# Performance work log

Measured on AMD Instinct MI355X. Metric: run time of the kernel, lower is better.

Reference implementation:

```python
import jax, jax.numpy as jnp
import numpy as np

N_MQ = 50000   # number of 'mq' (user/query) nodes
N_SQ = 50000   # number of 'sq' (movie/sub-query) nodes
E = 600000     # edges of type ('mq','queries','sq'); reverse edges are the flip
EL = 200000    # supervision edges for the classifier
H = 128        # hidden_channels
F_IN = 768     # raw 'sq' feature dim (movie_lin in_features)
N_LAYERS = 4


def setup_inputs() -> dict:
    key = jax.random.key(0)
    ks = jax.random.split(key, 12)
    sH = 1.0 / np.sqrt(H)
    sF = 1.0 / np.sqrt(F_IN)
    return {
        "mq_node_id": jnp.arange(N_MQ, dtype=jnp.int64) if jax.config.jax_enable_x64 else jnp.arange(N_MQ, dtype=jnp.int32),
        "sq_node_id": jnp.arange(N_SQ, dtype=jnp.int32),
        "sq_x": jax.random.normal(ks[0], (N_SQ, F_IN), jnp.float32),
        "edge_index": jax.random.randint(ks[1], (2, E), 0, N_SQ),
        "edge_label_index": jax.random.randint(ks[2], (2, EL), 0, N_SQ),
        "user_emb": jax.random.normal(ks[3], (N_MQ, H), jnp.float32) * 0.1,
        "movie_emb": jax.random.normal(ks[4], (N_SQ, H), jnp.float32) * 0.1,
        "lin_W": jax.random.normal(ks[5], (H, F_IN), jnp.float32) * sF,
        "lin_b": jnp.zeros((H,), jnp.float32),
        "Wl_s": jax.random.normal(ks[6], (N_LAYERS, H, H), jnp.float32) * sH,
        "bl_s": jnp.zeros((N_LAYERS, H), jnp.float32),
        "Wr_s": jax.random.normal(ks[7], (N_LAYERS, H, H), jnp.float32) * sH,
        "Wl_m": jax.random.normal(ks[8], (N_LAYERS, H, H), jnp.float32) * sH,
        "bl_m": jnp.zeros((N_LAYERS, H), jnp.float32),
        "Wr_m": jax.random.normal(ks[9], (N_LAYERS, H, H), jnp.float32) * sH,
    }


def _sage(x_src, x_dst, src_idx, dst_idx, Wl, bl, Wr, n_dst):
    """PyG SAGEConv (aggr='mean', root_weight=True, bias on lin_l only)."""
    msg = x_src[src_idx]                                     # [E, H] gather
    agg = jax.ops.segment_sum(msg, dst_idx, num_segments=n_dst)
    cnt = jax.ops.segment_sum(jnp.ones((src_idx.shape[0], 1), x_src.dtype),
                              dst_idx, num_segments=n_dst)
    mean = agg / jnp.maximum(cnt, 1.0)                       # mean over in-neighbors
    return mean @ Wl.T + bl + x_dst @ Wr.T


def reference(mq_node_id, sq_node_id, sq_x, edge_index, edge_label_index,
              user_emb, movie_emb, lin_W, lin_b,
              Wl_s, bl_s, Wr_s, Wl_m, bl_m, Wr_m):
    # input encoders
    x_mq = user_emb[mq_node_id]                              # [N_MQ, H]
    x_sq = sq_x @ lin_W.T + lin_b + movie_emb[sq_node_id]    # [N_SQ, H]
    src, dst = edge_index[0], edge_index[1]                  # mq -> sq; reverse is flip
    for i in range(N_LAYERS):
        new_sq = _sage(x_mq, x_sq, src, dst, Wl_s[i], bl_s[i], Wr_s[i], N_SQ)
        new_mq = _sage(x_sq, x_mq, dst, src, Wl_m[i], bl_m[i], Wr_m[i], N_MQ)
        if i == 0:  # only conv1 has ReLU in the original GNN
            new_sq = jax.nn.relu(new_sq)
            new_mq = jax.nn.relu(new_mq)
        x_mq, x_sq = new_mq, new_sq
    # dot-product classifier over supervision edges
    return (x_mq[edge_label_index[0]] * x_sq[edge_label_index[1]]).sum(axis=-1)
```

## Files before the change

### kernel.cpp

```cpp
#include <hip/hip_runtime.h>

#define H    128
#define NMQ  50000
#define NSQ  50000
#define NE   600000
#define NEL  200000
#define FIN  768
#define NLAYERS 4
#define NBLK (NSQ / 16)

typedef __attribute__((ext_vector_type(8))) short bf16x8;
typedef __attribute__((ext_vector_type(4))) float f32x4;

__device__ inline ushort f2b(float f) {
  unsigned u = __float_as_uint(f);
  u = (u + 0x7FFFu + ((u >> 16) & 1u)) >> 16;
  return (ushort)u;
}
__device__ inline float b2f(ushort h) { return __uint_as_float((unsigned)h << 16); }

__global__ void cvt_bf16(const float* __restrict__ in, ushort* __restrict__ out, int n4) {
  int i = blockIdx.x * blockDim.x + threadIdx.x;
  if (i >= n4) return;
  float4 v = ((const float4*)in)[i];
  ushort4 o;
  o.x = f2b(v.x); o.y = f2b(v.y); o.z = f2b(v.z); o.w = f2b(v.w);
  ((ushort4*)out)[i] = o;
}

__global__ void cvt_w5(const float* __restrict__ linW,
                       const float* __restrict__ Wls, const float* __restrict__ Wrs,
                       const float* __restrict__ Wlm, const float* __restrict__ Wrm,
                       ushort* olinW, ushort* oWls, ushort* oWrs, ushort* oWlm, ushort* oWrm) {
  const float* in; ushort* out; int n4;
  switch (blockIdx.y) {
    case 0: in = linW; out = olinW; n4 = H * FIN / 4; break;
    case 1: in = Wls;  out = oWls;  n4 = NLAYERS * H * H / 4; break;
    case 2: in = Wrs;  out = oWrs;  n4 = NLAYERS * H * H / 4; break;
    case 3: in = Wlm;  out = oWlm;  n4 = NLAYERS * H * H / 4; break;
    default: in = Wrm; out = oWrm;  n4 = NLAYERS * H * H / 4; break;
  }
  int i = blockIdx.x * blockDim.x + threadIdx.x;
  if (i >= n4) return;
  float4 v = ((const float4*)in)[i];
  ushort4 o;
  o.x = f2b(v.x); o.y = f2b(v.y); o.z = f2b(v.z); o.w = f2b(v.w);
  ((ushort4*)out)[i] = o;
}

__global__ __launch_bounds__(64) void encoder_mfma(
    const float* __restrict__ A, const ushort* __restrict__ Wb,
    const float* __restrict__ bias, const float* __restrict__ memb,
    ushort* __restrict__ C)
{
  int lane = threadIdx.x;
  int rowbase = blockIdx.x * 16;
  int t = lane >> 4, fr = lane & 15;
  f32x4 acc[8];
  #pragma unroll
  for (int c = 0; c < 8; ++c)
    #pragma unroll
    for (int q = 0; q < 4; ++q) acc[c][q] = 0.f;

  int arow = rowbase + fr;
  const float* Abase = A + (long)arow * FIN + t * 8;

  for (int k0 = 0; k0 < FIN; k0 += 32) {
    bf16x8 af, bfm[8];
    {
      const float* p = Abase + k0;
      float4 v0 = *(const float4*)p;
      float4 v1 = *(const float4*)(p + 4);
      ushort tmp[8];
      tmp[0] = f2b(v0.x); tmp[1] = f2b(v0.y); tmp[2] = f2b(v0.z); tmp[3] = f2b(v0.w);
      tmp[4] = f2b(v1.x); tmp[5] = f2b(v1.y); tmp[6] = f2b(v1.z); tmp[7] = f2b(v1.w);
      af = *(bf16x8*)tmp;
    }
    #pragma unroll
    for (int cc = 0; cc < 8; ++cc) {
      int col = cc * 16 + fr;
      bfm[cc] = *(const bf16x8*)(Wb + (long)col * FIN + k0 + t * 8);
    }
    #pragma unroll
    for (int cc = 0; cc < 8; ++cc)
      acc[cc] = __builtin_amdgcn_mfma_f32_16x16x32_bf16(af, bfm[cc], acc[cc], 0, 0, 0);
  }
  #pragma unroll
  for (int cc = 0; cc < 8; ++cc)
    #pragma unroll
    for (int q = 0; q < 4; ++q) {
      int row = rowbase + t * 4 + q;
      int col = cc * 16 + fr;
      float v = acc[cc][q] + bias[col] + memb[(long)row * H + col];
      C[(long)row * H + col] = f2b(v);
    }
}

__global__ __launch_bounds__(64) void fused_layer2(
    const ushort* __restrict__ xmq, const ushort* __restrict__ xsq,
    const int* __restrict__ offs_f, const int* __restrict__ csr_f,
    const int* __restrict__ offs_r, const int* __restrict__ csr_r,
    const ushort* __restrict__ Wls, const ushort* __restrict__ Wrs,
    const float* __restrict__ bls,
    const ushort* __restrict__ Wlm, const ushort* __restrict__ Wrm,
    const float* __restrict__ blm,
    ushort* __restrict__ nsq, ushort* __restrict__ nmq, int relu)
{
  __shared__ ushort mtile[16 * 128];
  int side = blockIdx.x >= NBLK;
  int bidx = side ? blockIdx.x - NBLK : blockIdx.x;
  const ushort* xg   = side ? xsq    : xmq;
  const ushort* xs   = side ? xmq    : xsq;
  const int*    offs = side ? offs_r : offs_f;
  const int*    csr  = side ? csr_r  : csr_f;
  const ushort* Wl   = side ? Wlm    : Wls;
  const ushort* Wr   = side ? Wrm    : Wrs;
  const float*  bias = side ? blm    : bls;
  ushort*       Cout = side ? nmq    : nsq;

  int lane = threadIdx.x;
  int rowbase = bidx * 16;
  int t = lane >> 4, fr = lane & 15;
  const unsigned* X = (const unsigned*)xg;

  int srow = rowbase + fr;
  bf16x8 sfrag[4];
  #pragma unroll
  for (int ks = 0; ks < 4; ++ks)
    sfrag[ks] = *(const bf16x8*)(xs + (long)srow * H + (ks * 4 + t) * 8);

  int wslot = lane >> 2;
  unsigned* mt32 = (unsigned*)mtile;
  for (int i = 0; i < 16; ++i) {
    int row = rowbase + i;
    int s = offs[row], e = offs[row + 1];
    float a0 = 0.f, a1 = 0.f;
    int j = s;
    for (; j + 8 <= e; j += 8) {
      long i0 = csr[j], i1 = csr[j+1], i2 = csr[j+2], i3 = csr[j+3];
      long i4 = csr[j+4], i5 = csr[j+5], i6 = csr[j+6], i7 = csr[j+7];
      unsigned x0 = X[i0*64+lane], x1 = X[i1*64+lane], x2 = X[i2*64+lane], x3 = X[i3*64+lane];
      unsigned x4 = X[i4*64+lane], x5 = X[i5*64+lane], x6 = X[i6*64+lane], x7 = X[i7*64+lane];
      a0 += b2f((ushort)(x0 & 0xffff)) + b2f((ushort)(x1 & 0xffff))
          + b2f((ushort)(x2 & 0xffff)) + b2f((ushort)(x3 & 0xffff))
          + b2f((ushort)(x4 & 0xffff)) + b2f((ushort)(x5 & 0xffff))
          + b2f((ushort)(x6 & 0xffff)) + b2f((ushort)(x7 & 0xffff));
      a1 += b2f((ushort)(x0 >> 16)) + b2f((ushort)(x1 >> 16))
          + b2f((ushort)(x2 >> 16)) + b2f((ushort)(x3 >> 16))
          + b2f((ushort)(x4 >> 16)) + b2f((ushort)(x5 >> 16))
          + b2f((ushort)(x6 >> 16)) + b2f((ushort)(x7 >> 16));
    }
    if (j + 4 <= e) {
      long i0 = csr[j], i1 = csr[j+1], i2 = csr[j+2], i3 = csr[j+3];
      unsigned x0 = X[i0*64+lane], x1 = X[i1*64+lane], x2 = X[i2*64+lane], x3 = X[i3*64+lane];
      a0 += b2f((ushort)(x0 & 0xffff)) + b2f((ushort)(x1 & 0xffff))
          + b2f((ushort)(x2 & 0xffff)) + b2f((ushort)(x3 & 0xffff));
      a1 += b2f((ushort)(x0 >> 16)) + b2f((ushort)(x1 >> 16))
          + b2f((ushort)(x2 >> 16)) + b2f((ushort)(x3 >> 16));
      j += 4;
    }
    for (; j < e; ++j) {
      unsigned x = X[(long)csr[j] * 64 + lane];
      a0 += b2f((ushort)(x & 0xffff));
      a1 += b2f((ushort)(x >> 16));
    }
    float inv = (e > s) ? 1.f / (float)(e - s) : 0.f;
    a0 *= inv; a1 *= inv;
    int sw = (wslot & 8) | ((wslot & 7) ^ (i & 7));
    mt32[i * 64 + sw * 4 + (lane & 3)] = (unsigned)f2b(a0) | ((unsigned)f2b(a1) << 16);
  }

  f32x4 acc[8];
  #pragma unroll
  for (int c = 0; c < 8; ++c)
    #pragma unroll
    for (int q = 0; q < 4; ++q) acc[c][q] = 0.f;

  #pragma unroll
  for (int ks = 0; ks < 4; ++ks) {
    int slot = ks * 4 + t;
    int sw = (slot & 8) | ((slot & 7) ^ (fr & 7));
    bf16x8 af = *(const bf16x8*)&mtile[fr * 128 + sw * 8];
    bf16x8 bfm[8];
    #pragma unroll
    for (int cc = 0; cc < 8; ++cc) {
      int col = cc * 16 + fr;
      bfm[cc] = *(const bf16x8*)(Wl + (long)col * H + slot * 8);
    }
    #pragma unroll
    for (int cc = 0; cc < 8; ++cc)
      acc[cc] = __builtin_amdgcn_mfma_f32_16x16x32_bf16(af, bfm[cc], acc[cc], 0, 0, 0);
  }
  #pragma unroll
  for (int ks = 0; ks < 4; ++ks) {
    int slot = ks * 4 + t;
    bf16x8 bfm[8];
    #pragma unroll
    for (int cc = 0; cc < 8; ++cc) {
      int col = cc * 16 + fr;
      bfm[cc] = *(const bf16x8*)(Wr + (long)col * H + slot * 8);
    }
    #pragma unroll
    for (int cc = 0; cc < 8; ++cc)
      acc[cc] = __builtin_amdgcn_mfma_f32_16x16x32_bf16(sfrag[ks], bfm[cc], acc[cc], 0, 0, 0);
  }
  #pragma unroll
  for (int cc = 0; cc < 8; ++cc)
    #pragma unroll
    for (int q = 0; q < 4; ++q) {
      int row = rowbase + t * 4 + q;
      int col = cc * 16 + fr;
      float v = acc[cc][q] + bias[col];
      if (relu) v = fmaxf(v, 0.f);
      Cout[(long)row * H + col] = f2b(v);
    }
}

__global__ void deg_count(const int* __restrict__ eidx, int* __restrict__ df, int* __restrict__ dr) {
  int e = blockIdx.x * blockDim.x + threadIdx.x;
  if (e >= NE) return;
  atomicAdd(dr + eidx[e], 1);
  atomicAdd(df + eidx[NE + e], 1);
}

__global__ __launch_bounds__(1024) void exscan2(
    const int* __restrict__ degf, const int* __restrict__ degr,
    int* __restrict__ offf, int* __restrict__ offr)
{
  __shared__ int part[1024];
  const int* deg = blockIdx.x ? degr : degf;
  int* offs = blockIdx.x ? offr : offf;
  int n = blockIdx.x ? NMQ : NSQ;
  int t = threadIdx.x;
  int chunk = (n + 1023) >> 10;
  int beg = t * chunk, end = beg + chunk;
  if (end > n) end = n;
  int s = 0;
  for (int i = beg; i < end; ++i) s += deg[i];
  part[t] = s;
  __syncthreads();
  for (int offd = 1; offd < 1024; offd <<= 1) {
    int v = 0;
    if (t >= offd) v = part[t - offd];
    __syncthreads();
    part[t] += v;
    __syncthreads();
  }
  int run = (t == 0) ? 0 : part[t - 1];
  for (int i = beg; i < end; ++i) { offs[i] = run; run += deg[i]; }
  if (t == 1023) offs[n] = part[1023];
}

__global__ void csr_fill(const int* __restrict__ eidx,
                         const int* __restrict__ offs_f, const int* __restrict__ offs_r,
                         int* __restrict__ cur_f, int* __restrict__ cur_r,
                         int* __restrict__ csr_f, int* __restrict__ csr_r) {
  int e = blockIdx.x * blockDim.x + threadIdx.x;
  if (e >= NE) return;
  int s = eidx[e], d = eidx[NE + e];
  int p = atomicAdd(cur_f + d, 1); csr_f[offs_f[d] + p] = s;
  int q = atomicAdd(cur_r + s, 1); csr_r[offs_r[s] + q] = d;
}

__global__ __launch_bounds__(256) void edge_dot_b(
    const ushort* __restrict__ xmq, const ushort* __restrict__ xsq,
    const int* __restrict__ eli, float* __restrict__ out)
{
  int wid = (blockIdx.x << 2) + (threadIdx.x >> 6);
  int lane = threadIdx.x & 63;
  if (wid >= NEL) return;
  int a = eli[wid], b = eli[NEL + wid];
  unsigned xa = ((const unsigned*)xmq)[(long)a * 64 + lane];
  unsigned xb = ((const unsigned*)xsq)[(long)b * 64 + lane];
  float p = b2f((ushort)(xa & 0xffff)) * b2f((ushort)(xb & 0xffff))
          + b2f((ushort)(xa >> 16))    * b2f((ushort)(xb >> 16));
  #pragma unroll
  for (int off = 32; off; off >>= 1) p += __shfl_down(p, off, 64);
  if (lane == 0) out[wid] = p;
}

extern "C" void kernel_launch(void* const* d_in, const int* in_sizes, int n_in,
                              void* d_out, int out_size, void* d_ws, size_t ws_size,
                              hipStream_t stream) {
  (void)in_sizes; (void)n_in; (void)out_size; (void)ws_size;
  const float* sq_x      = (const float*)d_in[2];
  const int*   eidx      = (const int*)d_in[3];
  const int*   eli       = (const int*)d_in[4];
  const float* user_emb  = (const float*)d_in[5];
  const float* movie_emb = (const float*)d_in[6];
  const float* lin_W     = (const float*)d_in[7];
  const float* lin_b     = (const float*)d_in[8];
  const float* Wl_s      = (const float*)d_in[9];
  const float* bl_s      = (const float*)d_in[10];
  const float* Wr_s      = (const float*)d_in[11];
  const float* Wl_m      = (const float*)d_in[12];
  const float* bl_m      = (const float*)d_in[13];
  const float* Wr_m      = (const float*)d_in[14];
  float* out = (float*)d_out;

  char* ws = (char*)d_ws;
  size_t off = 0;
  auto alloc = [&](size_t bytes) {
    char* p = ws + off;
    off += (bytes + 255) & ~(size_t)255;
    return p;
  };
  ushort* xmq_a = (ushort*)alloc((size_t)NMQ * H * 2);
  ushort* xmq_b = (ushort*)alloc((size_t)NMQ * H * 2);
  ushort* xsq_a = (ushort*)alloc((size_t)NSQ * H * 2);
  ushort* xsq_b = (ushort*)alloc((size_t)NSQ * H * 2);
  ushort* linWb = (ushort*)alloc((size_t)H * FIN * 2);
  ushort* Wlsb  = (ushort*)alloc((size_t)NLAYERS * H * H * 2);
  ushort* Wrsb  = (ushort*)alloc((size_t)NLAYERS * H * H * 2);
  ushort* Wlmb  = (ushort*)alloc((size_t)NLAYERS * H * H * 2);
  ushort* Wrmb  = (ushort*)alloc((size_t)NLAYERS * H * H * 2);
  int* deg_f  = (int*)alloc((size_t)NSQ * 4);
  int* deg_r  = (int*)alloc((size_t)NMQ * 4);
  int* cur_f  = (int*)alloc((size_t)NSQ * 4);
  int* cur_r  = (int*)alloc((size_t)NMQ * 4);
  int* offs_f = (int*)alloc((size_t)(NSQ + 1) * 4);
  int* offs_r = (int*)alloc((size_t)(NMQ + 1) * 4);
  int* csr_f  = (int*)alloc((size_t)NE * 4);
  int* csr_r  = (int*)alloc((size_t)NE * 4);

  hipMemsetAsync(deg_f, 0, (char*)offs_f - (char*)deg_f, stream);

  cvt_bf16<<<(NMQ * H / 4 + 255) / 256, 256, 0, stream>>>(user_emb, xmq_a, NMQ * H / 4);
  cvt_w5<<<dim3((H * FIN / 4 + 255) / 256, 5), 256, 0, stream>>>(
      lin_W, Wl_s, Wr_s, Wl_m, Wr_m, linWb, Wlsb, Wrsb, Wlmb, Wrmb);

  encoder_mfma<<<NSQ / 16, 64, 0, stream>>>(sq_x, linWb, lin_b, movie_emb, xsq_a);
  deg_count<<<(NE + 255) / 256, 256, 0, stream>>>(eidx, deg_f, deg_r);
  exscan2<<<2, 1024, 0, stream>>>(deg_f, deg_r, offs_f, offs_r);
  csr_fill<<<(NE + 255) / 256, 256, 0, stream>>>(eidx, offs_f, offs_r, cur_f, cur_r, csr_f, csr_r);

  ushort *cm = xmq_a, *cs = xsq_a, *nm = xmq_b, *ns = xsq_b;
  for (int l = 0; l < NLAYERS; ++l) {
    fused_layer2<<<2 * NBLK, 64, 0, stream>>>(cm, cs, offs_f, csr_f, offs_r, csr_r,
        Wlsb + (size_t)l * H * H, Wrsb + (size_t)l * H * H, bl_s + (size_t)l * H,
        Wlmb + (size_t)l * H * H, Wrmb + (size_t)l * H * H, bl_m + (size_t)l * H,
        ns, nm, l == 0);
    ushort* t;
    t = cm; cm = nm; nm = t;
    t = cs; cs = ns; ns = t;
  }
  edge_dot_b<<<(NEL + 3) / 4, 256, 0, stream>>>(cm, cs, eli, out);
}
```

Before: 724.8 us.

## Flatten block edge list and double-buffer neighbor gathers; prefetch encoder A loads

The per-row neighbor loop in the fused layer kernel is replaced by one flat pass over the block's whole CSR range. Gathers are issued 16 at a time into two alternating register buffers, and a new per-edge destination-row array tracks row boundaries and writes each row's mean when the row changes. This is meant to keep many independent loads in flight across row boundaries instead of stalling on rows with few neighbors, at the cost of extra register pressure and an extra array read per edge. The encoder also software-prefetches the next fp32 A fragment before each MFMA step.

```diff
diff --git a/kernel.cpp b/kernel.cpp
--- a/kernel.cpp
+++ b/kernel.cpp
@@ -63,28 +63,40 @@
     for (int q = 0; q < 4; ++q) acc[c][q] = 0.f;
 
   int arow = rowbase + fr;
-  const float* Abase = A + (long)arow * FIN + t * 8;
-
-  for (int k0 = 0; k0 < FIN; k0 += 32) {
-    bf16x8 af, bfm[8];
-    {
-      const float* p = Abase + k0;
-      float4 v0 = *(const float4*)p;
-      float4 v1 = *(const float4*)(p + 4);
-      ushort tmp[8];
-      tmp[0] = f2b(v0.x); tmp[1] = f2b(v0.y); tmp[2] = f2b(v0.z); tmp[3] = f2b(v0.w);
-      tmp[4] = f2b(v1.x); tmp[5] = f2b(v1.y); tmp[6] = f2b(v1.z); tmp[7] = f2b(v1.w);
-      af = *(bf16x8*)tmp;
-    }
-    #pragma unroll
-    for (int cc = 0; cc < 8; ++cc) {
-      int col = cc * 16 + fr;
-      bfm[cc] = *(const bf16x8*)(Wb + (long)col * FIN + k0 + t * 8);
-    }
-    #pragma unroll
-    for (int cc = 0; cc < 8; ++cc)
-      acc[cc] = __builtin_amdgcn_mfma_f32_16x16x32_bf16(af, bfm[cc], acc[cc], 0, 0, 0);
-  }
+  const float* Ab = A + (long)arow * FIN + t * 8;
+
+#define ENC_COMPUTE(k0, c0, c1) do {                                        \
+    ushort tmp[8];                                                          \
+    tmp[0] = f2b((c0).x); tmp[1] = f2b((c0).y);                             \
+    tmp[2] = f2b((c0).z); tmp[3] = f2b((c0).w);                             \
+    tmp[4] = f2b((c1).x); tmp[5] = f2b((c1).y);                             \
+    tmp[6] = f2b((c1).z); tmp[7] = f2b((c1).w);                             \
+    bf16x8 af = *(bf16x8*)tmp;                                              \
+    bf16x8 bfm[8];                                                          \
+    _Pragma("unroll")                                                       \
+    for (int cc = 0; cc < 8; ++cc) {                                        \
+      int col = cc * 16 + fr;                                               \
+      bfm[cc] = *(const bf16x8*)(Wb + (long)col * FIN + (k0) + t * 8);      \
+    }                                                                       \
+    _Pragma("unroll")                                                       \
+    for (int cc = 0; cc < 8; ++cc)                                          \
+      acc[cc] = __builtin_amdgcn_mfma_f32_16x16x32_bf16(af, bfm[cc], acc[cc], 0, 0, 0); \
+  } while (0)
+
+  float4 u0 = *(const float4*)Ab;
+  float4 u1 = *(const float4*)(Ab + 4);
+  for (int ki = 0; ki < FIN / 32; ki += 2) {
+    float4 v0 = *(const float4*)(Ab + (ki + 1) * 32);
+    float4 v1 = *(const float4*)(Ab + (ki + 1) * 32 + 4);
+    ENC_COMPUTE(ki * 32, u0, u1);
+    if (ki + 2 < FIN / 32) {
+      u0 = *(const float4*)(Ab + (ki + 2) * 32);
+      u1 = *(const float4*)(Ab + (ki + 2) * 32 + 4);
+    }
+    ENC_COMPUTE((ki + 1) * 32, v0, v1);
+  }
+#undef ENC_COMPUTE
+
   #pragma unroll
   for (int cc = 0; cc < 8; ++cc)
     #pragma unroll
@@ -99,7 +111,9 @@
 __global__ __launch_bounds__(64) void fused_layer2(
     const ushort* __restrict__ xmq, const ushort* __restrict__ xsq,
     const int* __restrict__ offs_f, const int* __restrict__ csr_f,
+    const int* __restrict__ drow_f,
     const int* __restrict__ offs_r, const int* __restrict__ csr_r,
+    const int* __restrict__ drow_r,
     const ushort* __restrict__ Wls, const ushort* __restrict__ Wrs,
     const float* __restrict__ bls,
     const ushort* __restrict__ Wlm, const ushort* __restrict__ Wrm,
@@ -113,6 +127,7 @@
   const ushort* xs   = side ? xmq    : xsq;
   const int*    offs = side ? offs_r : offs_f;
   const int*    csr  = side ? csr_r  : csr_f;
+  const int*    drow = side ? drow_r : drow_f;
   const ushort* Wl   = side ? Wlm    : Wls;
   const ushort* Wr   = side ? Wrm    : Wrs;
   const float*  bias = side ? blm    : bls;
@@ -131,44 +146,74 @@
 
   int wslot = lane >> 2;
   unsigned* mt32 = (unsigned*)mtile;
-  for (int i = 0; i < 16; ++i) {
-    int row = rowbase + i;
-    int s = offs[row], e = offs[row + 1];
-    float a0 = 0.f, a1 = 0.f;
-    int j = s;
-    for (; j + 8 <= e; j += 8) {
-      long i0 = csr[j], i1 = csr[j+1], i2 = csr[j+2], i3 = csr[j+3];
-      long i4 = csr[j+4], i5 = csr[j+5], i6 = csr[j+6], i7 = csr[j+7];
-      unsigned x0 = X[i0*64+lane], x1 = X[i1*64+lane], x2 = X[i2*64+lane], x3 = X[i3*64+lane];
-      unsigned x4 = X[i4*64+lane], x5 = X[i5*64+lane], x6 = X[i6*64+lane], x7 = X[i7*64+lane];
-      a0 += b2f((ushort)(x0 & 0xffff)) + b2f((ushort)(x1 & 0xffff))
-          + b2f((ushort)(x2 & 0xffff)) + b2f((ushort)(x3 & 0xffff))
-          + b2f((ushort)(x4 & 0xffff)) + b2f((ushort)(x5 & 0xffff))
-          + b2f((ushort)(x6 & 0xffff)) + b2f((ushort)(x7 & 0xffff));
-      a1 += b2f((ushort)(x0 >> 16)) + b2f((ushort)(x1 >> 16))
-          + b2f((ushort)(x2 >> 16)) + b2f((ushort)(x3 >> 16))
-          + b2f((ushort)(x4 >> 16)) + b2f((ushort)(x5 >> 16))
-          + b2f((ushort)(x6 >> 16)) + b2f((ushort)(x7 >> 16));
-    }
-    if (j + 4 <= e) {
-      long i0 = csr[j], i1 = csr[j+1], i2 = csr[j+2], i3 = csr[j+3];
-      unsigned x0 = X[i0*64+lane], x1 = X[i1*64+lane], x2 = X[i2*64+lane], x3 = X[i3*64+lane];
-      a0 += b2f((ushort)(x0 & 0xffff)) + b2f((ushort)(x1 & 0xffff))
-          + b2f((ushort)(x2 & 0xffff)) + b2f((ushort)(x3 & 0xffff));
-      a1 += b2f((ushort)(x0 >> 16)) + b2f((ushort)(x1 >> 16))
-          + b2f((ushort)(x2 >> 16)) + b2f((ushort)(x3 >> 16));
-      j += 4;
-    }
-    for (; j < e; ++j) {
-      unsigned x = X[(long)csr[j] * 64 + lane];
-      a0 += b2f((ushort)(x & 0xffff));
-      a1 += b2f((ushort)(x >> 16));
-    }
-    float inv = (e > s) ? 1.f / (float)(e - s) : 0.f;
-    a0 *= inv; a1 *= inv;
-    int sw = (wslot & 8) | ((wslot & 7) ^ (i & 7));
-    mt32[i * 64 + sw * 4 + (lane & 3)] = (unsigned)f2b(a0) | ((unsigned)f2b(a1) << 16);
-  }
+  #pragma unroll
+  for (int i = 0; i < 16; ++i) mt32[i * 64 + lane] = 0;
+
+  int cbeg = offs[rowbase], cend = offs[rowbase + 16];
+  float a0 = 0.f, a1 = 0.f;
+  int cur = -1, cnt = 0;
+
+#define GISSUE(ax, rx, c0, nn) do {                                         \
+    if ((nn) == 16) {                                                       \
+      _Pragma("unroll")                                                     \
+      for (int j = 0; j < 16; ++j) {                                        \
+        rx[j] = drow[(c0) + j];                                             \
+        ax[j] = X[(long)csr[(c0) + j] * 64 + lane];                         \
+      }                                                                     \
+    } else {                                                                \
+      _Pragma("unroll")                                                     \
+      for (int j = 0; j < 16; ++j) if (j < (nn)) {                          \
+        rx[j] = drow[(c0) + j];                                             \
+        ax[j] = X[(long)csr[(c0) + j] * 64 + lane];                         \
+      }                                                                     \
+    } } while (0)
+
+#define GCONSUME(ax, rx, nn) do {                                           \
+    _Pragma("unroll")                                                       \
+    for (int j = 0; j < 16; ++j) if (j < (nn)) {                            \
+      int rowj = rx[j];                                                     \
+      if (rowj != cur) {                                                    \
+        if (cnt > 0) {                                                      \
+          float inv = 1.f / (float)cnt;                                     \
+          int sw = (wslot & 8) | ((wslot & 7) ^ (cur & 7));                 \
+          mt32[(cur & 15) * 64 + sw * 4 + (lane & 3)] =                     \
+              (unsigned)f2b(a0 * inv) | ((unsigned)f2b(a1 * inv) << 16);    \
+        }                                                                   \
+        cur = rowj; a0 = 0.f; a1 = 0.f; cnt = 0;                            \
+      }                                                                     \
+      unsigned w = ax[j];                                                   \
+      a0 += b2f((ushort)(w & 0xffff));                                      \
+      a1 += b2f((ushort)(w >> 16));                                         \
+      ++cnt;                                                                \
+    } } while (0)
+
+  {
+    unsigned aA[16], aB[16];
+    int rA[16], rB[16];
+    int c = cbeg;
+    int nA = cend - c; if (nA > 16) nA = 16;
+    if (nA > 0) GISSUE(aA, rA, c, nA);
+    c += nA;
+    while (nA > 0) {
+      int nB = cend - c; if (nB > 16) nB = 16;
+      if (nB > 0) GISSUE(aB, rB, c, nB);
+      c += nB;
+      GCONSUME(aA, rA, nA);
+      if (nB == 0) break;
+      nA = cend - c; if (nA > 16) nA = 16;
+      if (nA > 0) GISSUE(aA, rA, c, nA);
+      c += nA;
+      GCONSUME(aB, rB, nB);
+    }
+    if (cnt > 0) {
+      float inv = 1.f / (float)cnt;
+      int sw = (wslot & 8) | ((wslot & 7) ^ (cur & 7));
+      mt32[(cur & 15) * 64 + sw * 4 + (lane & 3)] =
+          (unsigned)f2b(a0 * inv) | ((unsigned)f2b(a1 * inv) << 16);
+    }
+  }
+#undef GISSUE
+#undef GCONSUME
 
   f32x4 acc[8];
   #pragma unroll
@@ -254,12 +299,13 @@
 __global__ void csr_fill(const int* __restrict__ eidx,
                          const int* __restrict__ offs_f, const int* __restrict__ offs_r,
                          int* __restrict__ cur_f, int* __restrict__ cur_r,
-                         int* __restrict__ csr_f, int* __restrict__ csr_r) {
+                         int* __restrict__ csr_f, int* __restrict__ csr_r,
+                         int* __restrict__ drow_f, int* __restrict__ drow_r) {
   int e = blockIdx.x * blockDim.x + threadIdx.x;
   if (e >= NE) return;
   int s = eidx[e], d = eidx[NE + e];
-  int p = atomicAdd(cur_f + d, 1); csr_f[offs_f[d] + p] = s;
-  int q = atomicAdd(cur_r + s, 1); csr_r[offs_r[s] + q] = d;
+  int p = atomicAdd(cur_f + d, 1); int pf = offs_f[d] + p; csr_f[pf] = s; drow_f[pf] = d;
+  int q = atomicAdd(cur_r + s, 1); int pr = offs_r[s] + q; csr_r[pr] = d; drow_r[pr] = s;
 }
 
 __global__ __launch_bounds__(256) void edge_dot_b(
@@ -322,6 +368,8 @@
   int* offs_r = (int*)alloc((size_t)(NMQ + 1) * 4);
   int* csr_f  = (int*)alloc((size_t)NE * 4);
   int* csr_r  = (int*)alloc((size_t)NE * 4);
+  int* drow_f = (int*)alloc((size_t)NE * 4);
+  int* drow_r = (int*)alloc((size_t)NE * 4);
 
   hipMemsetAsync(deg_f, 0, (char*)offs_f - (char*)deg_f, stream);
 
@@ -332,11 +380,13 @@
   encoder_mfma<<<NSQ / 16, 64, 0, stream>>>(sq_x, linWb, lin_b, movie_emb, xsq_a);
   deg_count<<<(NE + 255) / 256, 256, 0, stream>>>(eidx, deg_f, deg_r);
   exscan2<<<2, 1024, 0, stream>>>(deg_f, deg_r, offs_f, offs_r);
-  csr_fill<<<(NE + 255) / 256, 256, 0, stream>>>(eidx, offs_f, offs_r, cur_f, cur_r, csr_f, csr_r);
+  csr_fill<<<(NE + 255) / 256, 256, 0, stream>>>(eidx, offs_f, offs_r, cur_f, cur_r,
+                                                 csr_f, csr_r, drow_f, drow_r);
 
   ushort *cm = xmq_a, *cs = xsq_a, *nm = xmq_b, *ns = xsq_b;
   for (int l = 0; l < NLAYERS; ++l) {
-    fused_layer2<<<2 * NBLK, 64, 0, stream>>>(cm, cs, offs_f, csr_f, offs_r, csr_r,
+    fused_layer2<<<2 * NBLK, 64, 0, stream>>>(cm, cs,
+        offs_f, csr_f, drow_f, offs_r, csr_r, drow_r,
         Wlsb + (size_t)l * H * H, Wrsb + (size_t)l * H * H, bl_s + (size_t)l * H,
         Wlmb + (size_t)l * H * H, Wrmb + (size_t)l * H * H, bl_m + (size_t)l * H,
         ns, nm, l == 0);
```

Result: faster. 700.8 us (-3.3%).

## Pack CSR into padded groups of four and gather with 16-lane vector loads

Applied to the files above, without the earlier changes.

Changes the CSR build so each destination's neighbor list is padded into groups of four slots, with a group-to-row array. The aggregation loop then processes a block's 16 rows as one stream of groups. Each quarter-wave gathers a full 256-byte row with bf16x8 loads, the loads are double-buffered across banks of four groups, and partial sums are reduced with cross-lane shuffles. This targets the per-row serial loop and the 4-byte-per-lane gathers. In exchange it adds padding work for masked slots, a second scan, extra memset and metadata buffers, and a fixed NGMAX capacity that depends on the degree distribution.

```diff
diff --git a/kernel.cpp b/kernel.cpp
--- a/kernel.cpp
+++ b/kernel.cpp
@@ -8,6 +8,8 @@
 #define FIN  768
 #define NLAYERS 4
 #define NBLK (NSQ / 16)
+#define NGMAX 188000
+#define PCMAX (NGMAX * 4)
 
 typedef __attribute__((ext_vector_type(8))) short bf16x8;
 typedef __attribute__((ext_vector_type(4))) float f32x4;
@@ -68,9 +70,9 @@
   for (int k0 = 0; k0 < FIN; k0 += 32) {
     bf16x8 af, bfm[8];
     {
-      const float* p = Abase + k0;
-      float4 v0 = *(const float4*)p;
-      float4 v1 = *(const float4*)(p + 4);
+      const float* pp = Abase + k0;
+      float4 v0 = *(const float4*)pp;
+      float4 v1 = *(const float4*)(pp + 4);
       ushort tmp[8];
       tmp[0] = f2b(v0.x); tmp[1] = f2b(v0.y); tmp[2] = f2b(v0.z); tmp[3] = f2b(v0.w);
       tmp[4] = f2b(v1.x); tmp[5] = f2b(v1.y); tmp[6] = f2b(v1.z); tmp[7] = f2b(v1.w);
@@ -98,8 +100,10 @@
 
 __global__ __launch_bounds__(64) void fused_layer2(
     const ushort* __restrict__ xmq, const ushort* __restrict__ xsq,
-    const int* __restrict__ offs_f, const int* __restrict__ csr_f,
-    const int* __restrict__ offs_r, const int* __restrict__ csr_r,
+    const int* __restrict__ offs_f, const int* __restrict__ goff_f,
+    const int* __restrict__ pcsr_f, const int* __restrict__ grow_f,
+    const int* __restrict__ offs_r, const int* __restrict__ goff_r,
+    const int* __restrict__ pcsr_r, const int* __restrict__ grow_r,
     const ushort* __restrict__ Wls, const ushort* __restrict__ Wrs,
     const float* __restrict__ bls,
     const ushort* __restrict__ Wlm, const ushort* __restrict__ Wrm,
@@ -112,63 +116,99 @@
   const ushort* xg   = side ? xsq    : xmq;
   const ushort* xs   = side ? xmq    : xsq;
   const int*    offs = side ? offs_r : offs_f;
-  const int*    csr  = side ? csr_r  : csr_f;
+  const int*    goff = side ? goff_r : goff_f;
+  const int*    pcsr = side ? pcsr_r : pcsr_f;
+  const int*    grow = side ? grow_r : grow_f;
   const ushort* Wl   = side ? Wlm    : Wls;
   const ushort* Wr   = side ? Wrm    : Wrs;
   const float*  bias = side ? blm    : bls;
   ushort*       Cout = side ? nmq    : nsq;
 
   int lane = threadIdx.x;
+  int ep = lane >> 4;
+  int ch = lane & 15;
   int rowbase = bidx * 16;
+
   int t = lane >> 4, fr = lane & 15;
-  const unsigned* X = (const unsigned*)xg;
-
   int srow = rowbase + fr;
   bf16x8 sfrag[4];
   #pragma unroll
   for (int ks = 0; ks < 4; ++ks)
     sfrag[ks] = *(const bf16x8*)(xs + (long)srow * H + (ks * 4 + t) * 8);
 
-  int wslot = lane >> 2;
   unsigned* mt32 = (unsigned*)mtile;
-  for (int i = 0; i < 16; ++i) {
-    int row = rowbase + i;
-    int s = offs[row], e = offs[row + 1];
-    float a0 = 0.f, a1 = 0.f;
-    int j = s;
-    for (; j + 8 <= e; j += 8) {
-      long i0 = csr[j], i1 = csr[j+1], i2 = csr[j+2], i3 = csr[j+3];
-      long i4 = csr[j+4], i5 = csr[j+5], i6 = csr[j+6], i7 = csr[j+7];
-      unsigned x0 = X[i0*64+lane], x1 = X[i1*64+lane], x2 = X[i2*64+lane], x3 = X[i3*64+lane];
-      unsigned x4 = X[i4*64+lane], x5 = X[i5*64+lane], x6 = X[i6*64+lane], x7 = X[i7*64+lane];
-      a0 += b2f((ushort)(x0 & 0xffff)) + b2f((ushort)(x1 & 0xffff))
-          + b2f((ushort)(x2 & 0xffff)) + b2f((ushort)(x3 & 0xffff))
-          + b2f((ushort)(x4 & 0xffff)) + b2f((ushort)(x5 & 0xffff))
-          + b2f((ushort)(x6 & 0xffff)) + b2f((ushort)(x7 & 0xffff));
-      a1 += b2f((ushort)(x0 >> 16)) + b2f((ushort)(x1 >> 16))
-          + b2f((ushort)(x2 >> 16)) + b2f((ushort)(x3 >> 16))
-          + b2f((ushort)(x4 >> 16)) + b2f((ushort)(x5 >> 16))
-          + b2f((ushort)(x6 >> 16)) + b2f((ushort)(x7 >> 16));
-    }
-    if (j + 4 <= e) {
-      long i0 = csr[j], i1 = csr[j+1], i2 = csr[j+2], i3 = csr[j+3];
-      unsigned x0 = X[i0*64+lane], x1 = X[i1*64+lane], x2 = X[i2*64+lane], x3 = X[i3*64+lane];
-      a0 += b2f((ushort)(x0 & 0xffff)) + b2f((ushort)(x1 & 0xffff))
-          + b2f((ushort)(x2 & 0xffff)) + b2f((ushort)(x3 & 0xffff));
-      a1 += b2f((ushort)(x0 >> 16)) + b2f((ushort)(x1 >> 16))
-          + b2f((ushort)(x2 >> 16)) + b2f((ushort)(x3 >> 16));
-      j += 4;
-    }
-    for (; j < e; ++j) {
-      unsigned x = X[(long)csr[j] * 64 + lane];
-      a0 += b2f((ushort)(x & 0xffff));
-      a1 += b2f((ushort)(x >> 16));
-    }
-    float inv = (e > s) ? 1.f / (float)(e - s) : 0.f;
-    a0 *= inv; a1 *= inv;
-    int sw = (wslot & 8) | ((wslot & 7) ^ (i & 7));
-    mt32[i * 64 + sw * 4 + (lane & 3)] = (unsigned)f2b(a0) | ((unsigned)f2b(a1) << 16);
-  }
+  #pragma unroll
+  for (int i = 0; i < 16; ++i) mt32[i * 64 + lane] = 0;
+
+  float acc8[8];
+  #pragma unroll
+  for (int q = 0; q < 8; ++q) acc8[q] = 0.f;
+  int cur = -1;
+
+  int gbeg = goff[rowbase], gend = goff[rowbase + 16];
+  int gn = gend - gbeg;
+
+#define FLUSH() do {                                                        \
+    if (cur >= 0) {                                                         \
+      _Pragma("unroll")                                                     \
+      for (int q = 0; q < 8; ++q) {                                         \
+        acc8[q] += __shfl_xor(acc8[q], 16, 64);                             \
+        acc8[q] += __shfl_xor(acc8[q], 32, 64);                             \
+      }                                                                     \
+      int s0 = offs[cur], e0 = offs[cur + 1];                               \
+      float inv = (e0 > s0) ? 1.f / (float)(e0 - s0) : 0.f;                 \
+      if (ep == 0) {                                                        \
+        ushort tmp[8];                                                      \
+        _Pragma("unroll")                                                   \
+        for (int q = 0; q < 8; ++q) tmp[q] = f2b(acc8[q] * inv);            \
+        int sw = (ch & 8) | ((ch & 7) ^ (cur & 7));                         \
+        *(bf16x8*)&mtile[(cur & 15) * 128 + sw * 8] = *(bf16x8*)tmp;        \
+      }                                                                     \
+      _Pragma("unroll")                                                     \
+      for (int q = 0; q < 8; ++q) acc8[q] = 0.f;                            \
+    } } while (0)
+
+#define LOADBANK(vv, mm, rr, g0) do {                                       \
+    _Pragma("unroll")                                                       \
+    for (int k = 0; k < 4; ++k) {                                           \
+      int gg = (g0) + k;                                                    \
+      int ggs = gg < gend ? gg : gbeg;                                      \
+      int si = pcsr[ggs * 4 + ep];                                          \
+      mm[k] = si >= 0 ? 1.f : 0.f;                                          \
+      long rsafe = si >= 0 ? si : 0;                                        \
+      vv[k] = *(const bf16x8*)(xg + rsafe * H + ch * 8);                    \
+      rr[k] = grow[ggs];                                                    \
+    } } while (0)
+
+#define CONSUMEBANK(vv, mm, rr, g0) do {                                    \
+    _Pragma("unroll")                                                       \
+    for (int k = 0; k < 4; ++k) {                                           \
+      int gg = (g0) + k;                                                    \
+      if (gg < gend) {                                                      \
+        int rnow = rr[k];                                                   \
+        if (rnow != cur) { FLUSH(); cur = rnow; }                           \
+        _Pragma("unroll")                                                   \
+        for (int q = 0; q < 8; ++q)                                         \
+          acc8[q] = fmaf(mm[k], b2f((ushort)vv[k][q]), acc8[q]);            \
+      }                                                                     \
+    } } while (0)
+
+  if (gn > 0) {
+    bf16x8 vA[4], vB[4];
+    float mA[4], mB[4];
+    int rA[4], rB[4];
+    LOADBANK(vA, mA, rA, gbeg);
+    for (int base = 0; base < gn; base += 8) {
+      LOADBANK(vB, mB, rB, gbeg + base + 4);
+      CONSUMEBANK(vA, mA, rA, gbeg + base);
+      LOADBANK(vA, mA, rA, gbeg + base + 8);
+      CONSUMEBANK(vB, mB, rB, gbeg + base + 4);
+    }
+    FLUSH();
+  }
+#undef FLUSH
+#undef LOADBANK
+#undef CONSUMEBANK
 
   f32x4 acc[8];
   #pragma unroll
@@ -225,41 +265,70 @@
 
 __global__ __launch_bounds__(1024) void exscan2(
     const int* __restrict__ degf, const int* __restrict__ degr,
-    int* __restrict__ offf, int* __restrict__ offr)
+    int* __restrict__ offf, int* __restrict__ offr,
+    int* __restrict__ gofff, int* __restrict__ goffr)
 {
   __shared__ int part[1024];
   const int* deg = blockIdx.x ? degr : degf;
   int* offs = blockIdx.x ? offr : offf;
+  int* goffs = blockIdx.x ? goffr : gofff;
   int n = blockIdx.x ? NMQ : NSQ;
   int t = threadIdx.x;
   int chunk = (n + 1023) >> 10;
   int beg = t * chunk, end = beg + chunk;
   if (end > n) end = n;
-  int s = 0;
-  for (int i = beg; i < end; ++i) s += deg[i];
-  part[t] = s;
+
+  {
+    int s = 0;
+    for (int i = beg; i < end; ++i) s += deg[i];
+    part[t] = s;
+    __syncthreads();
+    for (int offd = 1; offd < 1024; offd <<= 1) {
+      int v = 0;
+      if (t >= offd) v = part[t - offd];
+      __syncthreads();
+      part[t] += v;
+      __syncthreads();
+    }
+    int run = (t == 0) ? 0 : part[t - 1];
+    for (int i = beg; i < end; ++i) { offs[i] = run; run += deg[i]; }
+    if (t == 1023) offs[n] = part[1023];
+  }
   __syncthreads();
-  for (int offd = 1; offd < 1024; offd <<= 1) {
-    int v = 0;
-    if (t >= offd) v = part[t - offd];
+  {
+    int s = 0;
+    for (int i = beg; i < end; ++i) s += (deg[i] + 3) >> 2;
+    part[t] = s;
     __syncthreads();
-    part[t] += v;
-    __syncthreads();
-  }
-  int run = (t == 0) ? 0 : part[t - 1];
-  for (int i = beg; i < end; ++i) { offs[i] = run; run += deg[i]; }
-  if (t == 1023) offs[n] = part[1023];
+    for (int offd = 1; offd < 1024; offd <<= 1) {
+      int v = 0;
+      if (t >= offd) v = part[t - offd];
+      __syncthreads();
+      part[t] += v;
+      __syncthreads();
+    }
+    int run = (t == 0) ? 0 : part[t - 1];
+    for (int i = beg; i < end; ++i) { goffs[i] = run; run += (deg[i] + 3) >> 2; }
+    if (t == 1023) goffs[n] = part[1023];
+  }
 }
 
 __global__ void csr_fill(const int* __restrict__ eidx,
-                         const int* __restrict__ offs_f, const int* __restrict__ offs_r,
+                         const int* __restrict__ goff_f, const int* __restrict__ goff_r,
                          int* __restrict__ cur_f, int* __restrict__ cur_r,
-                         int* __restrict__ csr_f, int* __restrict__ csr_r) {
+                         int* __restrict__ pcsr_f, int* __restrict__ pcsr_r,
+                         int* __restrict__ grow_f, int* __restrict__ grow_r) {
   int e = blockIdx.x * blockDim.x + threadIdx.x;
   if (e >= NE) return;
   int s = eidx[e], d = eidx[NE + e];
-  int p = atomicAdd(cur_f + d, 1); csr_f[offs_f[d] + p] = s;
-  int q = atomicAdd(cur_r + s, 1); csr_r[offs_r[s] + q] = d;
+  int p = atomicAdd(cur_f + d, 1);
+  int g = goff_f[d] + (p >> 2);
+  pcsr_f[g * 4 + (p & 3)] = s;
+  grow_f[g] = d;
+  int q = atomicAdd(cur_r + s, 1);
+  int g2 = goff_r[s] + (q >> 2);
+  pcsr_r[g2 * 4 + (q & 3)] = d;
+  grow_r[g2] = s;
 }
 
 __global__ __launch_bounds__(256) void edge_dot_b(
@@ -320,10 +389,15 @@
   int* cur_r  = (int*)alloc((size_t)NMQ * 4);
   int* offs_f = (int*)alloc((size_t)(NSQ + 1) * 4);
   int* offs_r = (int*)alloc((size_t)(NMQ + 1) * 4);
-  int* csr_f  = (int*)alloc((size_t)NE * 4);
-  int* csr_r  = (int*)alloc((size_t)NE * 4);
+  int* goff_f = (int*)alloc((size_t)(NSQ + 1) * 4);
+  int* goff_r = (int*)alloc((size_t)(NMQ + 1) * 4);
+  int* pcsr_f = (int*)alloc((size_t)PCMAX * 4);
+  int* pcsr_r = (int*)alloc((size_t)PCMAX * 4);
+  int* grow_f = (int*)alloc((size_t)NGMAX * 4);
+  int* grow_r = (int*)alloc((size_t)NGMAX * 4);
 
   hipMemsetAsync(deg_f, 0, (char*)offs_f - (char*)deg_f, stream);
+  hipMemsetAsync(pcsr_f, 0xFF, (char*)grow_f - (char*)pcsr_f, stream);
 
   cvt_bf16<<<(NMQ * H / 4 + 255) / 256, 256, 0, stream>>>(user_emb, xmq_a, NMQ * H / 4);
   cvt_w5<<<dim3((H * FIN / 4 + 255) / 256, 5), 256, 0, stream>>>(
@@ -331,12 +405,15 @@
 
   encoder_mfma<<<NSQ / 16, 64, 0, stream>>>(sq_x, linWb, lin_b, movie_emb, xsq_a);
   deg_count<<<(NE + 255) / 256, 256, 0, stream>>>(eidx, deg_f, deg_r);
-  exscan2<<<2, 1024, 0, stream>>>(deg_f, deg_r, offs_f, offs_r);
-  csr_fill<<<(NE + 255) / 256, 256, 0, stream>>>(eidx, offs_f, offs_r, cur_f, cur_r, csr_f, csr_r);
+  exscan2<<<2, 1024, 0, stream>>>(deg_f, deg_r, offs_f, offs_r, goff_f, goff_r);
+  csr_fill<<<(NE + 255) / 256, 256, 0, stream>>>(eidx, goff_f, goff_r, cur_f, cur_r,
+                                                 pcsr_f, pcsr_r, grow_f, grow_r);
 
   ushort *cm = xmq_a, *cs = xsq_a, *nm = xmq_b, *ns = xsq_b;
   for (int l = 0; l < NLAYERS; ++l) {
-    fused_layer2<<<2 * NBLK, 64, 0, stream>>>(cm, cs, offs_f, csr_f, offs_r, csr_r,
+    fused_layer2<<<2 * NBLK, 64, 0, stream>>>(cm, cs,
+        offs_f, goff_f, pcsr_f, grow_f,
+        offs_r, goff_r, pcsr_r, grow_r,
         Wlsb + (size_t)l * H * H, Wrsb + (size_t)l * H * H, bl_s + (size_t)l * H,
         Wlmb + (size_t)l * H * H, Wrmb + (size_t)l * H * H, bl_m + (size_t)l * H,
         ns, nm, l == 0);
```

Result: slower. 763.6 us (+5.4%).
